# Kernel optimization log

Measured on AMD Instinct MI355X. Metric: run time of the kernel, lower is better.

The kernel has to match this reference:

```python
import jax, jax.numpy as jnp
import numpy as np

NUM_PHRASE = 8
HDIM = 256
NUM_HEADS = 8
NUM_LAYERS = 3
MIN_DIST = 2


def sine_pos(mask, num_feats, temperature=10000.0):
    # PositionEmbeddingSine (1D, DETR-style, normalize=False)
    B, L = mask.shape
    x_embed = jnp.cumsum(mask.astype(jnp.float32), axis=1)            # [B,L]
    dim_t = jnp.arange(num_feats, dtype=jnp.float32)
    dim_t = temperature ** (2.0 * jnp.floor(dim_t / 2.0) / num_feats)
    pos = x_embed[:, :, None] / dim_t                                  # [B,L,C]
    pos = jnp.stack([jnp.sin(pos[:, :, 0::2]), jnp.cos(pos[:, :, 1::2])], axis=3)
    return pos.reshape(B, L, num_feats)


def layer_norm(x, g, b, eps=1e-5):
    mu = jnp.mean(x, axis=-1, keepdims=True)
    var = jnp.mean((x - mu) ** 2, axis=-1, keepdims=True)
    return (x - mu) / jnp.sqrt(var + eps) * g + b


def mha(q, k, v, key_mask, in_w, in_b, out_w, out_b, nheads):
    # torch nn.MultiheadAttention (batch_first, eval/no-dropout), averaged attn weights
    B, Lq, C = q.shape
    Dh = C // nheads
    qp = (q @ in_w[:, :C] + in_b[:C]).reshape(B, Lq, nheads, Dh)
    kp = (k @ in_w[:, C:2 * C] + in_b[C:2 * C]).reshape(B, -1, nheads, Dh)
    vp = (v @ in_w[:, 2 * C:] + in_b[2 * C:]).reshape(B, -1, nheads, Dh)
    scores = jnp.einsum('bqhd,bkhd->bhqk', qp, kp) / jnp.sqrt(jnp.float32(Dh))
    scores = jnp.where(key_mask[:, None, None, :], scores, -jnp.inf)
    attn = jax.nn.softmax(scores, axis=-1)
    out = jnp.einsum('bhqk,bkhd->bqhd', attn, vp).reshape(B, Lq, C)
    return out @ out_w + out_b, jnp.mean(attn, axis=1)


def cross_attention(x, y, mask, qw, qb, kvw, kvb, inw, inb, ow, ob, g0, b0, lw, lb, g1, b1):
    C = x.shape[-1]
    q = x @ qw + qb
    kv = y @ kvw + kvb
    k, v = kv[..., :C], kv[..., C:]
    q_att, attn = mha(q, k, v, mask, inw, inb, ow, ob, NUM_HEADS)
    x = layer_norm(x + q_att, g0, b0)
    update = jax.nn.relu(x @ lw + lb)
    x = layer_norm(x + update, g1, b1)
    return x, attn


def _select_one(entropy_b, mask_b):
    # greedy highest-entropy selection with min-distance suppression (1D NMS)
    P, MD = NUM_PHRASE, MIN_DIST
    score = jnp.where(mask_b, entropy_b, -jnp.inf)
    order = jnp.argsort(-score).astype(jnp.int32)   # valid indices first, descending entropy

    def step(carry, idx):
        sel, cnt = carry
        dists = jnp.where(sel >= 0, jnp.abs(idx - sel), 1000000)
        ok = mask_b[idx] & (cnt < P) & (jnp.min(dists) >= MD)
        new_sel = jnp.where(ok, sel.at[jnp.minimum(cnt, P - 1)].set(idx), sel)
        return (new_sel, cnt + ok.astype(jnp.int32)), None

    init = (jnp.full((P,), -1, jnp.int32), jnp.int32(0))
    (sel, cnt), _ = jax.lax.scan(step, init, order)
    last = sel[jnp.maximum(cnt - 1, 0)]
    return jnp.where(jnp.arange(P) < cnt, sel, last)   # pad by repeating last


def phrase_generate(txt_emb, txt_mask, video_feats, video_mask,
                    word_proj_w, word_proj_b, video_proj_w, video_proj_b,
                    q_w, q_b, kv_w, kv_b, in_w, in_b, out_w, out_b,
                    ln0_g, ln0_b, lin_w, lin_b, ln1_g, ln1_b, eos_slot):
    B, L, C = txt_emb.shape
    word_emb = txt_emb[:, 1:]
    word_mask = txt_mask[:, 1:]
    word_pe = word_emb + sine_pos(word_mask, C)

    # word importance via video cross-attention entropy
    wp = word_pe @ word_proj_w + word_proj_b                      # [B,Lw,C]
    vp = video_feats @ video_proj_w + video_proj_b                # [B,T,C]
    sim = jnp.einsum('blc,btc->blt', wp, vp)                      # [B,Lw,T]
    sim = jnp.where(video_mask[:, None, :], sim, -jnp.inf)
    attn_weights = jax.nn.softmax(sim, axis=2)
    entropy = -jnp.sum(attn_weights * jnp.log(attn_weights + 1e-6), axis=2)  # [B,Lw]

    sel = jax.vmap(_select_one)(entropy, word_mask)               # [B,P] int32
    phrase_slot = jnp.take_along_axis(word_pe, sel[:, :, None], axis=1)      # [B,P,C]

    slot_sim = None
    for i in range(NUM_LAYERS):
        phrase_slot, slot_sim = cross_attention(
            phrase_slot, word_pe, word_mask,
            q_w[i], q_b[i], kv_w[i], kv_b[i], in_w[i], in_b[i], out_w[i], out_b[i],
            ln0_g[i], ln0_b[i], lin_w[i], lin_b[i], ln1_g[i], ln1_b[i])

    eos = jnp.broadcast_to(eos_slot, (B, 1, C))
    return phrase_slot, attn_weights, slot_sim, eos


def setup_inputs() -> dict:
    key = jax.random.key(0)
    ks = jax.random.split(key, 16)
    B, L, T, C, NL = 128, 257, 1024, HDIM, NUM_LAYERS
    s = 0.02
    inp = {
        'txt_emb': jax.random.normal(ks[0], (B, L, C), jnp.float32),
        'txt_mask': jnp.ones((B, L), jnp.bool_),
        'video_feats': jax.random.normal(ks[1], (B, T, C), jnp.float32),
        'video_mask': jnp.ones((B, T), jnp.bool_),
        'word_proj_w': jax.random.normal(ks[2], (C, C)) * s,
        'word_proj_b': jnp.zeros((C,)),
        'video_proj_w': jax.random.normal(ks[3], (C, C)) * s,
        'video_proj_b': jnp.zeros((C,)),
        'q_w': jax.random.normal(ks[4], (NL, C, C)) * s,
        'q_b': jnp.zeros((NL, C)),
        'kv_w': jax.random.normal(ks[5], (NL, C, 2 * C)) * s,
        'kv_b': jnp.zeros((NL, 2 * C)),
        'in_w': jax.random.normal(ks[6], (NL, C, 3 * C)) * s,
        'in_b': jnp.zeros((NL, 3 * C)),
        'out_w': jax.random.normal(ks[7], (NL, C, C)) * s,
        'out_b': jnp.zeros((NL, C)),
        'ln0_g': jnp.ones((NL, C)),
        'ln0_b': jnp.zeros((NL, C)),
        'lin_w': jax.random.normal(ks[8], (NL, C, C)) * s,
        'lin_b': jnp.zeros((NL, C)),
        'ln1_g': jnp.ones((NL, C)),
        'ln1_b': jnp.zeros((NL, C)),
        'eos_slot': jax.random.normal(ks[9], (1, 1, C)),
    }
    return inp


def reference(txt_emb, txt_mask, video_feats, video_mask,
              word_proj_w, word_proj_b, video_proj_w, video_proj_b,
              q_w, q_b, kv_w, kv_b, in_w, in_b, out_w, out_b,
              ln0_g, ln0_b, lin_w, lin_b, ln1_g, ln1_b, eos_slot):
    return phrase_generate(txt_emb, txt_mask, video_feats, video_mask,
                           word_proj_w, word_proj_b, video_proj_w, video_proj_b,
                           q_w, q_b, kv_w, kv_b, in_w, in_b, out_w, out_b,
                           ln0_g, ln0_b, lin_w, lin_b, ln1_g, ln1_b, eos_slot)
```

## Files before the change

kernel.cpp:

```cpp
#include <hip/hip_runtime.h>
#include <math.h>

#define BB 128
#define LFULL 257
#define LW 256
#define TT 1024
#define CC 256
#define NH 8
#define DHD 32
#define PP 8
#define NLAY 3

typedef __bf16 bf16x8 __attribute__((ext_vector_type(8)));
typedef __bf16 bf16x4 __attribute__((ext_vector_type(4)));
typedef float  f32x4  __attribute__((ext_vector_type(4)));

__device__ __forceinline__ float blockReduceSum(float v, volatile float* lds) {
#pragma unroll
    for (int m = 32; m >= 1; m >>= 1) v += __shfl_xor(v, m);
    __syncthreads();
    if ((threadIdx.x & 63) == 0) lds[threadIdx.x >> 6] = v;
    __syncthreads();
    return lds[0] + lds[1] + lds[2] + lds[3];
}
__device__ __forceinline__ float blockReduceMax(float v, volatile float* lds) {
#pragma unroll
    for (int m = 32; m >= 1; m >>= 1) v = fmaxf(v, __shfl_xor(v, m));
    __syncthreads();
    if ((threadIdx.x & 63) == 0) lds[threadIdx.x >> 6] = v;
    __syncthreads();
    return fmaxf(fmaxf(lds[0], lds[1]), fmaxf(lds[2], lds[3]));
}


__device__ __forceinline__ int ldsoff(int row, int col) {
    return ((row >> 6) << 11)
         + ((((row >> 4) & 3) << 2) + (col >> 3)) * 128
         + ((row & 15) << 3) + (col & 7);
}

template<int SPLIT, int B_F32, int OUT_SPLIT>
__global__ __launch_bounds__(256) void gemm_mfma(
    const __bf16* __restrict__ Ahi, const __bf16* __restrict__ Alo, int lda, long long sA,
    const void* __restrict__ Bhp, const void* __restrict__ Blp, int ldb, long long sB,
    const float* __restrict__ bias,
    float* __restrict__ Cf, __bf16* __restrict__ Chi, __bf16* __restrict__ Clo,
    int ldc, long long sC, int M, int N, int K)
{
    __shared__ __bf16 sAh[4096];
    __shared__ __bf16 sAl[SPLIT ? 4096 : 1];
    __shared__ __bf16 sBh[4096];
    __shared__ __bf16 sBl[SPLIT ? 4096 : 1];

    const int tid = threadIdx.x;
    const int n0 = blockIdx.x * 128;
    const int m0 = blockIdx.y * 128;
    const long long bz = blockIdx.z;
    const __bf16* Ah = Ahi + bz * sA;
    const __bf16* Al = SPLIT ? (Alo + bz * sA) : nullptr;

    const int wv = tid >> 6, lane = tid & 63;
    const int wm = (wv & 1) << 6, wn = (wv >> 1) << 6;
    const int lr = lane & 15, quad = lane >> 4;

    const int sr = tid >> 2;
    const int sc = (tid & 3) << 3;
    const int fr = tid >> 3;
    const int fc = (tid & 7) << 2;

    const int abase = ((wm >> 6) << 11) + (lane << 3);
    const int bbase = ((wn >> 6) << 11) + (lane << 3);

    f32x4 acc[4][4];
#pragma unroll
    for (int i = 0; i < 4; ++i)
#pragma unroll
        for (int j = 0; j < 4; ++j) acc[i][j] = (f32x4)(0.f);

    for (int k0 = 0; k0 < K; k0 += 32) {
#pragma unroll
        for (int j = 0; j < 2; ++j) {
            int row = sr + 64 * j;
            int off = ldsoff(row, sc);
            *(bf16x8*)&sAh[off] =
                *(const bf16x8*)&Ah[(long long)(m0 + row) * lda + k0 + sc];
            if constexpr (SPLIT)
                *(bf16x8*)&sAl[off] =
                    *(const bf16x8*)&Al[(long long)(m0 + row) * lda + k0 + sc];
        }
        if constexpr (B_F32) {
            const float* Bf = (const float*)Bhp + bz * sB;
#pragma unroll
            for (int j = 0; j < 4; ++j) {
                int row = fr + 32 * j;
                float4 f = *(const float4*)&Bf[(long long)(n0 + row) * ldb + k0 + fc];
                bf16x4 h4, l4;
                h4[0] = (__bf16)f.x; l4[0] = (__bf16)(f.x - (float)h4[0]);
                h4[1] = (__bf16)f.y; l4[1] = (__bf16)(f.y - (float)h4[1]);
                h4[2] = (__bf16)f.z; l4[2] = (__bf16)(f.z - (float)h4[2]);
                h4[3] = (__bf16)f.w; l4[3] = (__bf16)(f.w - (float)h4[3]);
                int off = ldsoff(row, fc);
                *(bf16x4*)&sBh[off] = h4;
                *(bf16x4*)&sBl[off] = l4;
            }
        } else {
            const __bf16* Bh = (const __bf16*)Bhp + bz * sB;
#pragma unroll
            for (int j = 0; j < 2; ++j) {
                int row = sr + 64 * j;
                int off = ldsoff(row, sc);
                *(bf16x8*)&sBh[off] =
                    *(const bf16x8*)&Bh[(long long)(n0 + row) * ldb + k0 + sc];
                if constexpr (SPLIT) {
                    const __bf16* Bl = (const __bf16*)Blp + bz * sB;
                    *(bf16x8*)&sBl[off] =
                        *(const bf16x8*)&Bl[(long long)(n0 + row) * ldb + k0 + sc];
                }
            }
        }
        __syncthreads();

        bf16x8 fah[4], fbh[4];
        bf16x8 fal[4], fbl[4];
#pragma unroll
        for (int i = 0; i < 4; ++i) {
            fah[i] = *(const bf16x8*)&sAh[abase + i * 512];
            fbh[i] = *(const bf16x8*)&sBh[bbase + i * 512];
            if constexpr (SPLIT) {
                fal[i] = *(const bf16x8*)&sAl[abase + i * 512];
                fbl[i] = *(const bf16x8*)&sBl[bbase + i * 512];
            }
        }
#pragma unroll
        for (int i = 0; i < 4; ++i)
#pragma unroll
            for (int j = 0; j < 4; ++j) {
                if constexpr (SPLIT) {
                    acc[i][j] = __builtin_amdgcn_mfma_f32_16x16x32_bf16(fal[i], fbh[j], acc[i][j], 0, 0, 0);
                    acc[i][j] = __builtin_amdgcn_mfma_f32_16x16x32_bf16(fah[i], fbl[j], acc[i][j], 0, 0, 0);
                }
                acc[i][j] = __builtin_amdgcn_mfma_f32_16x16x32_bf16(fah[i], fbh[j], acc[i][j], 0, 0, 0);
            }
        __syncthreads();
    }

#pragma unroll
    for (int i = 0; i < 4; ++i)
#pragma unroll
        for (int j = 0; j < 4; ++j) {
            int col = n0 + wn + j * 16 + lr;
            int row0 = m0 + wm + i * 16 + quad * 4;
            float bv = bias ? bias[col] : 0.f;
#pragma unroll
            for (int r = 0; r < 4; ++r) {
                float v = acc[i][j][r] + bv;
                long long off = (long long)(row0 + r) * ldc + col + bz * sC;
                if constexpr (OUT_SPLIT) {
                    __bf16 h = (__bf16)v;
                    Chi[off] = h;
                    Clo[off] = (__bf16)(v - (float)h);
                } else {
                    Cf[off] = v;
                }
            }
        }
}

#define GTS 64
#define GKT 16
#define GPAD 68

template<int TRANSB, int RELU, int TRANSC>
__global__ __launch_bounds__(256) void gemm_f32(
    const float* __restrict__ A, int lda, long long sA,
    const float* __restrict__ Bm, int ldb, long long sB,
    const float* __restrict__ bias,
    float* __restrict__ C, int ldc, long long sC,
    int M, int N, int K)
{
    __shared__ float As[GKT][GPAD];
    __shared__ float Bs[GKT][GPAD];
    const int tid = threadIdx.x;
    const int tx = tid & 15, ty = tid >> 4;
    const int n0 = blockIdx.x * GTS;
    const int m0 = blockIdx.y * GTS;
    const long long bz = blockIdx.z;
    const float* Ab = A + bz * sA;
    const float* Bb = Bm + bz * sB;
    float* Cb = C + bz * sC;

    const int lr = tid >> 2;
    const int lc = (tid & 3) << 2;
    const int br = tid >> 4;
    const int bc = (tid & 15) << 2;

    float acc[4][4] = {};

    for (int k0 = 0; k0 < K; k0 += GKT) {
        float4 a = *(const float4*)&Ab[(long long)(m0 + lr) * lda + k0 + lc];
        As[lc + 0][lr] = a.x; As[lc + 1][lr] = a.y;
        As[lc + 2][lr] = a.z; As[lc + 3][lr] = a.w;
        if (TRANSB) {
            float4 b = *(const float4*)&Bb[(long long)(n0 + lr) * ldb + k0 + lc];
            Bs[lc + 0][lr] = b.x; Bs[lc + 1][lr] = b.y;
            Bs[lc + 2][lr] = b.z; Bs[lc + 3][lr] = b.w;
        } else {
            float4 b = *(const float4*)&Bb[(long long)(k0 + br) * ldb + n0 + bc];
            *(float4*)&Bs[br][bc] = b;
        }
        __syncthreads();
#pragma unroll
        for (int k = 0; k < GKT; ++k) {
            float4 av = *(const float4*)&As[k][ty << 2];
            float4 bv = *(const float4*)&Bs[k][tx << 2];
            float ar[4] = {av.x, av.y, av.z, av.w};
            float brr[4] = {bv.x, bv.y, bv.z, bv.w};
#pragma unroll
            for (int i = 0; i < 4; ++i)
#pragma unroll
                for (int j = 0; j < 4; ++j)
                    acc[i][j] = fmaf(ar[i], brr[j], acc[i][j]);
        }
        __syncthreads();
    }

    float bbr[4] = {0.f, 0.f, 0.f, 0.f};
    if (bias) {
        float4 bb = *(const float4*)&bias[n0 + (tx << 2)];
        bbr[0] = bb.x; bbr[1] = bb.y; bbr[2] = bb.z; bbr[3] = bb.w;
    }
#pragma unroll
    for (int i = 0; i < 4; ++i) {
#pragma unroll
        for (int j = 0; j < 4; ++j) {
            float o = acc[i][j] + bbr[j];
            if (RELU) o = fmaxf(o, 0.f);
            if (TRANSC)
                Cb[(long long)(n0 + (tx << 2) + j) * ldc + m0 + (ty << 2) + i] = o;
            else
                Cb[(long long)(m0 + (ty << 2) + i) * ldc + n0 + (tx << 2) + j] = o;
        }
    }
}


__global__ __launch_bounds__(256) void cumsum_kernel(
    const int* __restrict__ tm, int* __restrict__ cums)
{
    int b = blockIdx.x, c = threadIdx.x;
    int lane = c & 63;
    int v = (tm[(long long)b * LFULL + 1 + c] != 0) ? 1 : 0;
#pragma unroll
    for (int off = 1; off < 64; off <<= 1) {
        int t = __shfl_up(v, off);
        if (lane >= off) v += t;
    }
    __shared__ int wsum[4];
    if (lane == 63) wsum[c >> 6] = v;
    __syncthreads();
    int w = c >> 6, add = 0;
    for (int i = 0; i < w; ++i) add += wsum[i];
    cums[b * LW + c] = v + add;
}

__global__ __launch_bounds__(256) void pe_table_kernel(float* __restrict__ petab)
{
    int n = blockIdx.x;
    int c = threadIdx.x;
    int i2 = c & ~1;
    float freq = powf(10000.0f, (float)i2 / (float)CC);
    float arg = (float)n / freq;
    petab[n * CC + c] = (c & 1) ? cosf(arg) : sinf(arg);
}

__global__ __launch_bounds__(256) void word_pe2_kernel(
    const float* __restrict__ te, const int* __restrict__ cums,
    const float* __restrict__ petab,
    __bf16* __restrict__ whi, __bf16* __restrict__ wlo)
{
    int g = blockIdx.x * 256 + threadIdx.x;
    int c0 = (g & 63) << 2;
    int l  = (g >> 6) & 255;
    int b  = g >> 14;
    int cnt = cums[b * LW + l];
    float4 s = *(const float4*)&te[((long long)(b * LFULL + 1 + l)) * CC + c0];
    float4 p = *(const float4*)&petab[cnt * CC + c0];
    float v0 = s.x + p.x, v1 = s.y + p.y, v2 = s.z + p.z, v3 = s.w + p.w;
    bf16x4 h, lo;
    h[0] = (__bf16)v0; lo[0] = (__bf16)(v0 - (float)h[0]);
    h[1] = (__bf16)v1; lo[1] = (__bf16)(v1 - (float)h[1]);
    h[2] = (__bf16)v2; lo[2] = (__bf16)(v2 - (float)h[2]);
    h[3] = (__bf16)v3; lo[3] = (__bf16)(v3 - (float)h[3]);
    long long o = ((long long)(b * LW + l)) * CC + c0;
    *(bf16x4*)&whi[o] = h;
    *(bf16x4*)&wlo[o] = lo;
}

__global__ __launch_bounds__(256) void split_transpose_kernel(
    const float* __restrict__ W, __bf16* __restrict__ hi, __bf16* __restrict__ lo)
{
    int n = blockIdx.x, k = threadIdx.x;
    float v = W[(long long)k * CC + n];
    __bf16 h = (__bf16)v;
    hi[(long long)n * CC + k] = h;
    lo[(long long)n * CC + k] = (__bf16)(v - (float)h);
}
__global__ __launch_bounds__(256) void split_plain_kernel(
    const float* __restrict__ W, __bf16* __restrict__ hi, __bf16* __restrict__ lo)
{
    int g = blockIdx.x * 256 + threadIdx.x;
    float v = W[g];
    __bf16 h = (__bf16)v;
    hi[g] = h;
    lo[g] = (__bf16)(v - (float)h);
}
__global__ __launch_bounds__(256) void cvt_bf16_kernel(
    const float* __restrict__ src, __bf16* __restrict__ dst)
{
    int g = blockIdx.x * 256 + threadIdx.x;
    dst[g] = (__bf16)src[g];
}

__global__ __launch_bounds__(256) void softmax_entropy_kernel(
    float* __restrict__ attn, const int* __restrict__ vmask,
    float* __restrict__ ent)
{
    __shared__ float lds[4];
    long long row = blockIdx.x;
    int b = blockIdx.x >> 8;
    float* p = attn + row * TT;
    const int* m = vmask + (long long)b * TT;
    int t4 = threadIdx.x * 4;
    float4 v = *(const float4*)&p[t4];
    int4 mm4 = *(const int4*)&m[t4];
    float x[4];
    x[0] = mm4.x ? v.x : -INFINITY;
    x[1] = mm4.y ? v.y : -INFINITY;
    x[2] = mm4.z ? v.z : -INFINITY;
    x[3] = mm4.w ? v.w : -INFINITY;
    float mx = fmaxf(fmaxf(x[0], x[1]), fmaxf(x[2], x[3]));
    mx = blockReduceMax(mx, lds);
    float e[4];
    float ps = 0.f;
#pragma unroll
    for (int j = 0; j < 4; ++j) { e[j] = expf(x[j] - mx); ps += e[j]; }
    float sum = blockReduceSum(ps, lds);
    float q[4];
    float ce = 0.f;
#pragma unroll
    for (int j = 0; j < 4; ++j) {
        q[j] = e[j] / sum;
        ce += q[j] * logf(q[j] + 1e-6f);
    }
    ce = blockReduceSum(ce, lds);
    *(float4*)&p[t4] = make_float4(q[0], q[1], q[2], q[3]);
    if (threadIdx.x == 0) ent[row] = -ce;
}

__global__ __launch_bounds__(256) void select_kernel(
    const float* __restrict__ ent, const int* __restrict__ tm,
    int* __restrict__ sel)
{
    int b = blockIdx.x;
    int l = threadIdx.x;
    __shared__ float sc[LW];
    __shared__ int ord[LW];
    __shared__ unsigned char mk[LW];
    mk[l] = (tm[(long long)b * LFULL + 1 + l] != 0);
    sc[l] = mk[l] ? ent[(long long)b * LW + l] : -INFINITY;
    __syncthreads();
    float mys = sc[l];
    int r = 0;
    for (int j = 0; j < LW; ++j) {
        float s = sc[j];
        r += (s > mys) || (s == mys && j < l);
    }
    ord[r] = l;
    __syncthreads();
    if (l == 0) {
        int chosen[PP];
        int cnt = 0;
        for (int t = 0; t < LW; ++t) {
            int idx = ord[t];
            if (!mk[idx]) continue;
            if (cnt >= PP) break;
            bool ok = true;
            for (int s2 = 0; s2 < cnt; ++s2) {
                int d = idx - chosen[s2];
                if (d < 0) d = -d;
                if (d < 2) ok = false;
            }
            if (ok) chosen[cnt++] = idx;
        }
        int last = (cnt > 0) ? chosen[cnt - 1] : -1;
        for (int p = 0; p < PP; ++p)
            sel[b * PP + p] = (p < cnt) ? chosen[p] : last;
    }
}

__global__ __launch_bounds__(256) void gather_kernel(
    const __bf16* __restrict__ whi, const __bf16* __restrict__ wlo,
    const int* __restrict__ sel, float* __restrict__ x0)
{
    int g = blockIdx.x * 256 + threadIdx.x;
    int b = g >> 11;
    int p = (g >> 8) & 7;
    int c = g & 255;
    int idx = sel[b * PP + p];
    if (idx < 0) idx = 0;
    long long off = ((long long)b * LW + idx) * CC + c;
    x0[g] = (float)whi[off] + (float)wlo[off];
}

__global__ __launch_bounds__(256) void eff_bias_kernel(
    const float* __restrict__ q_b, const float* __restrict__ kv_b,
    const float* __restrict__ in_w, const float* __restrict__ in_b,
    float* __restrict__ BQE_all, float* __restrict__ bkv3)
{
    int i = blockIdx.x / 3;
    int role = blockIdx.x % 3;
    int n = threadIdx.x;
    const float* inw = in_w + (long long)i * 196608;
    const float* inb = in_b + (long long)i * 768;
    const float* srcb;
    int co;
    float* dst;
    if (role == 0)      { srcb = q_b + i * 256;        co = 0;   dst = BQE_all + i * 256; }
    else if (role == 1) { srcb = kv_b + i * 512;       co = 256; dst = bkv3 + i * 512; }
    else                { srcb = kv_b + i * 512 + 256; co = 512; dst = bkv3 + i * 512 + 256; }
    float s = inb[co + n];
    for (int k = 0; k < CC; ++k)
        s = fmaf(srcb[k], inw[(long long)k * 768 + co + n], s);
    dst[n] = s;
}

__global__ __launch_bounds__(256) void attn_scores_kernel(
    const float* __restrict__ qp, const float* __restrict__ KV,
    const int* __restrict__ tm, float* __restrict__ attn)
{
    int b = blockIdx.x, h = blockIdx.y;
    int tid = threadIdx.x;
    __shared__ float qs[PP][DHD];
    __shared__ float sc[PP][LW];
    __shared__ float mxs[PP], sms[PP];
    {
        int q = tid >> 5, d = tid & 31;
        qs[q][d] = qp[((long long)(b * PP + q)) * CC + h * DHD + d];
    }
    __syncthreads();
    const float* kr = KV + ((long long)(b * LW + tid)) * 512 + h * DHD;
    float kreg[DHD];
#pragma unroll
    for (int j = 0; j < 8; ++j) {
        float4 f = *(const float4*)&kr[j * 4];
        kreg[j * 4 + 0] = f.x; kreg[j * 4 + 1] = f.y;
        kreg[j * 4 + 2] = f.z; kreg[j * 4 + 3] = f.w;
    }
    bool mk = tm[(long long)b * LFULL + 1 + tid] != 0;
#pragma unroll
    for (int q = 0; q < PP; ++q) {
        float s = 0.f;
#pragma unroll
        for (int d = 0; d < DHD; ++d) s = fmaf(qs[q][d], kreg[d], s);
        sc[q][tid] = mk ? s * 0.17677669529663687f : -INFINITY;
    }
    __syncthreads();
    {
        int q = tid >> 5, j = tid & 31;
        float m = -INFINITY;
        for (int kk = j; kk < LW; kk += 32) m = fmaxf(m, sc[q][kk]);
#pragma unroll
        for (int mm = 16; mm >= 1; mm >>= 1) m = fmaxf(m, __shfl_xor(m, mm, 32));
        float s = 0.f;
        for (int kk = j; kk < LW; kk += 32) s += expf(sc[q][kk] - m);
#pragma unroll
        for (int mm = 16; mm >= 1; mm >>= 1) s += __shfl_xor(s, mm, 32);
        if (j == 0) { mxs[q] = m; sms[q] = s; }
    }
    __syncthreads();
#pragma unroll
    for (int q = 0; q < PP; ++q) {
        float pv = expf(sc[q][tid] - mxs[q]) / sms[q];
        attn[(((long long)(b * NH + h)) * PP + q) * LW + tid] = pv;
    }
}

__global__ __launch_bounds__(256) void attn_out_kernel(
    const float* __restrict__ attn, const float* __restrict__ KV,
    float* __restrict__ aout)
{
    int b = blockIdx.x, q = blockIdx.y;
    int c = threadIdx.x, h = c >> 5;
    __shared__ float att[NH][LW];
#pragma unroll
    for (int hh = 0; hh < NH; ++hh)
        att[hh][c] = attn[(((long long)(b * NH + hh)) * PP + q) * LW + c];
    __syncthreads();
    const float* vpb = KV + ((long long)b * LW) * 512 + 256 + c;
    float acc = 0.f;
#pragma unroll 8
    for (int k = 0; k < LW; ++k)
        acc = fmaf(att[h][k], vpb[(long long)k * 512], acc);
    aout[((long long)(b * PP + q)) * CC + c] = acc;
}

__global__ __launch_bounds__(256) void slot_sim_kernel(
    const float* __restrict__ attn, float* __restrict__ outs)
{
    int b = blockIdx.x, q = blockIdx.y, k = threadIdx.x;
    float s = 0.f;
#pragma unroll
    for (int h = 0; h < NH; ++h)
        s += attn[(((long long)(b * NH + h)) * PP + q) * LW + k];
    outs[((long long)(b * PP + q)) * LW + k] = s * 0.125f;
}

__global__ __launch_bounds__(256) void ln_residual_kernel(
    const float* __restrict__ xin, const float* __restrict__ add,
    const float* __restrict__ g, const float* __restrict__ bta,
    float* __restrict__ out)
{
    __shared__ float lds[4];
    int r = blockIdx.x, c = threadIdx.x;
    long long idx = (long long)r * CC + c;
    float v = xin[idx] + add[idx];
    float s = blockReduceSum(v, lds);
    float mu = s * (1.0f / (float)CC);
    float d = v - mu;
    float var = blockReduceSum(d * d, lds) * (1.0f / (float)CC);
    out[idx] = d / sqrtf(var + 1e-5f) * g[c] + bta[c];
}

__global__ __launch_bounds__(256) void eos_kernel(
    const float* __restrict__ eos, float* __restrict__ outp)
{
    outp[(long long)blockIdx.x * CC + threadIdx.x] = eos[threadIdx.x];
}

extern "C" void kernel_launch(void* const* d_in, const int* in_sizes, int n_in,
                              void* d_out, int out_size, void* d_ws, size_t ws_size,
                              hipStream_t stream) {
    const float* txt_emb     = (const float*)d_in[0];
    const int*   txt_mask    = (const int*)d_in[1];
    const float* video_feats = (const float*)d_in[2];
    const int*   video_mask  = (const int*)d_in[3];
    const float* word_proj_w = (const float*)d_in[4];
    const float* word_proj_b = (const float*)d_in[5];
    const float* video_proj_w = (const float*)d_in[6];
    const float* q_w   = (const float*)d_in[8];
    const float* q_b   = (const float*)d_in[9];
    const float* kv_w  = (const float*)d_in[10];
    const float* kv_b  = (const float*)d_in[11];
    const float* in_w  = (const float*)d_in[12];
    const float* in_b  = (const float*)d_in[13];
    const float* out_w = (const float*)d_in[14];
    const float* out_b = (const float*)d_in[15];
    const float* ln0_g = (const float*)d_in[16];
    const float* ln0_b = (const float*)d_in[17];
    const float* lin_w = (const float*)d_in[18];
    const float* lin_b = (const float*)d_in[19];
    const float* ln1_g = (const float*)d_in[20];
    const float* ln1_b = (const float*)d_in[21];
    const float* eos_slot = (const float*)d_in[22];

    float* ws = (float*)d_ws;
    __bf16* wpe_hi = (__bf16*)(ws + 0LL);
    __bf16* wpe_lo = (__bf16*)(ws + 4194304LL);
    __bf16* wp_hi  = (__bf16*)(ws + 8388608LL);
    __bf16* wp_lo  = (__bf16*)(ws + 12582912LL);
    __bf16* U_hi   = (__bf16*)(ws + 16777216LL);
    __bf16* U_lo   = (__bf16*)(ws + 20971520LL);
    float*  KV     = ws + 8388608LL;
    float* ent     = ws + 25165824LL;
    int*   sel     = (int*)(ws + 25198592LL);
    float* x0      = ws + 25199616LL;
    float* x1      = ws + 25461760LL;
    float* xmid    = ws + 25723904LL;
    float* qp      = ws + 25986048LL;
    float* attnw   = ws + 26248192LL;
    float* aout    = ws + 28345344LL;
    float* qatt    = ws + 28607488LL;
    float* upd     = ws + 28869632LL;
    float* WQE_all = ws + 29131776LL;
    float* BQE_all = ws + 29328384LL;
    float* WT3f    = ws + 29329152LL;
    __bf16* WT3    = (__bf16*)(ws + 29722368LL);
    float* bkv3    = ws + 29918976LL;
    __bf16* WPT_hi = (__bf16*)(ws + 29920512LL);
    __bf16* WPT_lo = (__bf16*)(ws + 29953280LL);
    __bf16* VPS_hi = (__bf16*)(ws + 29986048LL);
    __bf16* VPS_lo = (__bf16*)(ws + 30018816LL);

    int*   cums  = (int*)(ws + 8388608LL);
    float* petab = ws + 8421376LL;

    float* outp     = (float*)d_out;
    float* out_ps   = outp;
    float* out_attn = outp + 262144LL;
    float* out_slot = outp + 33816576LL;
    float* out_eos  = outp + 34078720LL;

    cumsum_kernel<<<dim3(BB), dim3(256), 0, stream>>>(txt_mask, cums);
    pe_table_kernel<<<dim3(257), dim3(256), 0, stream>>>(petab);
    word_pe2_kernel<<<dim3(8192), dim3(256), 0, stream>>>(txt_emb, cums, petab, wpe_hi, wpe_lo);
    split_transpose_kernel<<<dim3(256), dim3(256), 0, stream>>>(word_proj_w, WPT_hi, WPT_lo);
    split_plain_kernel<<<dim3(256), dim3(256), 0, stream>>>(video_proj_w, VPS_hi, VPS_lo);
    gemm_mfma<1,0,1><<<dim3(2,256,1), dim3(256), 0, stream>>>(
        wpe_hi, wpe_lo, 256, 0, WPT_hi, WPT_lo, 256, 0, word_proj_b,
        nullptr, wp_hi, wp_lo, 256, 0, 32768, 256, 256);
    gemm_mfma<1,0,1><<<dim3(2,256,1), dim3(256), 0, stream>>>(
        wp_hi, wp_lo, 256, 0, VPS_hi, VPS_lo, 256, 0, nullptr,
        nullptr, U_hi, U_lo, 256, 0, 32768, 256, 256);
    gemm_mfma<1,1,0><<<dim3(8,2,BB), dim3(256), 0, stream>>>(
        U_hi, U_lo, 256, 65536LL, video_feats, nullptr, 256, 262144LL, nullptr,
        out_attn, nullptr, nullptr, 1024, 262144LL, 256, 1024, 256);
    softmax_entropy_kernel<<<dim3(32768), dim3(256), 0, stream>>>(out_attn, video_mask, ent);
    select_kernel<<<dim3(BB), dim3(256), 0, stream>>>(ent, txt_mask, sel);
    gather_kernel<<<dim3(1024), dim3(256), 0, stream>>>(wpe_hi, wpe_lo, sel, x0);

    gemm_f32<0,0,0><<<dim3(4,4,3), dim3(256), 0, stream>>>(
        q_w,256,65536LL, in_w,768,196608LL, nullptr, WQE_all,256,65536LL, 256,256,256);
    gemm_f32<0,0,1><<<dim3(4,4,3), dim3(256), 0, stream>>>(
        kv_w,512,131072LL, in_w+256,768,196608LL, nullptr, WT3f,256,131072LL, 256,256,256);
    gemm_f32<0,0,1><<<dim3(4,4,3), dim3(256), 0, stream>>>(
        kv_w+256,512,131072LL, in_w+512,768,196608LL, nullptr, WT3f+65536,256,131072LL, 256,256,256);
    eff_bias_kernel<<<dim3(9), dim3(256), 0, stream>>>(q_b, kv_b, in_w, in_b, BQE_all, bkv3);
    cvt_bf16_kernel<<<dim3(1536), dim3(256), 0, stream>>>(WT3f, (__bf16*)WT3);

    float* X = x0;
    for (int i = 0; i < NLAY; ++i) {
        const float* ow  = out_w + (long long)i * 65536;
        const float* ob  = out_b + (long long)i * 256;
        const float* g0  = ln0_g + (long long)i * 256;
        const float* b0  = ln0_b + (long long)i * 256;
        const float* lw  = lin_w + (long long)i * 65536;
        const float* lb  = lin_b + (long long)i * 256;
        const float* g1  = ln1_g + (long long)i * 256;
        const float* b1  = ln1_b + (long long)i * 256;

        gemm_mfma<0,0,0><<<dim3(4,256,1), dim3(256), 0, stream>>>(
            wpe_hi, nullptr, 256, 0, WT3 + (long long)i * 131072, nullptr, 256, 0,
            bkv3 + i * 512, KV, nullptr, nullptr, 512, 0, 32768, 512, 256);

        gemm_f32<0,0,0><<<dim3(4,16,1), dim3(256), 0, stream>>>(
            X,256,0, WQE_all + (long long)i*65536,256,0, BQE_all + i*256, qp,256,0, 1024,256,256);

        attn_scores_kernel<<<dim3(BB,NH), dim3(256), 0, stream>>>(qp, KV, txt_mask, attnw);
        attn_out_kernel<<<dim3(BB,PP), dim3(256), 0, stream>>>(attnw, KV, aout);
        if (i == NLAY - 1)
            slot_sim_kernel<<<dim3(BB,PP), dim3(256), 0, stream>>>(attnw, out_slot);

        gemm_f32<0,0,0><<<dim3(4,16,1), dim3(256), 0, stream>>>(
            aout,256,0, ow,256,0, ob, qatt,256,0, 1024,256,256);
        ln_residual_kernel<<<dim3(1024), dim3(256), 0, stream>>>(X, qatt, g0, b0, xmid);
        gemm_f32<0,1,0><<<dim3(4,16,1), dim3(256), 0, stream>>>(
            xmid,256,0, lw,256,0, lb, upd,256,0, 1024,256,256);
        float* Xout = (i == NLAY - 1) ? out_ps : ((X == x0) ? x1 : x0);
        ln_residual_kernel<<<dim3(1024), dim3(256), 0, stream>>>(xmid, upd, g1, b1, Xout);
        X = Xout;
    }
    eos_kernel<<<dim3(BB), dim3(256), 0, stream>>>(eos_slot, out_eos);
}
```

Baseline: 914.9 us.

## Use 512-thread blocks in MFMA GEMM with 8 waves per 128x128 tile

The bf16 MFMA GEMM now launches 512 threads per block, so 8 waves each compute a 64x32 sub-tile instead of 4 waves each computing 64x64. Each thread loads one row-chunk of A and B per k-step instead of two, and the fp32 B path converts 8 values per thread. The goal is more waves in flight to hide latency and a smaller per-thread accumulator and register footprint. The trade-off is more barrier participants and a lower MFMA-to-LDS-read ratio per wave.

Measured after the change: 894.1 us. -2.3%, faster.

```diff
diff --git a/kernel.cpp b/kernel.cpp
--- a/kernel.cpp
+++ b/kernel.cpp
@@ -40,7 +40,7 @@
 }
 
 template<int SPLIT, int B_F32, int OUT_SPLIT>
-__global__ __launch_bounds__(256) void gemm_mfma(
+__global__ __launch_bounds__(512, 4) void gemm_mfma(
     const __bf16* __restrict__ Ahi, const __bf16* __restrict__ Alo, int lda, long long sA,
     const void* __restrict__ Bhp, const void* __restrict__ Blp, int ldb, long long sB,
     const float* __restrict__ bias,
@@ -60,81 +60,79 @@
     const __bf16* Al = SPLIT ? (Alo + bz * sA) : nullptr;
 
     const int wv = tid >> 6, lane = tid & 63;
-    const int wm = (wv & 1) << 6, wn = (wv >> 1) << 6;
+    const int wm = (wv & 1) << 6;
+    const int wn = (wv >> 1) << 5;
     const int lr = lane & 15, quad = lane >> 4;
 
     const int sr = tid >> 2;
     const int sc = (tid & 3) << 3;
-    const int fr = tid >> 3;
-    const int fc = (tid & 7) << 2;
 
     const int abase = ((wm >> 6) << 11) + (lane << 3);
-    const int bbase = ((wn >> 6) << 11) + (lane << 3);
-
-    f32x4 acc[4][4];
+    const int bbase = ((wn >> 6) << 11) + (((wn >> 4) & 3) << 9) + (lane << 3);
+
+    f32x4 acc[4][2];
 #pragma unroll
     for (int i = 0; i < 4; ++i)
 #pragma unroll
-        for (int j = 0; j < 4; ++j) acc[i][j] = (f32x4)(0.f);
+        for (int j = 0; j < 2; ++j) acc[i][j] = (f32x4)(0.f);
 
     for (int k0 = 0; k0 < K; k0 += 32) {
-#pragma unroll
-        for (int j = 0; j < 2; ++j) {
-            int row = sr + 64 * j;
-            int off = ldsoff(row, sc);
+        {
+            int off = ldsoff(sr, sc);
             *(bf16x8*)&sAh[off] =
-                *(const bf16x8*)&Ah[(long long)(m0 + row) * lda + k0 + sc];
+                *(const bf16x8*)&Ah[(long long)(m0 + sr) * lda + k0 + sc];
             if constexpr (SPLIT)
                 *(bf16x8*)&sAl[off] =
-                    *(const bf16x8*)&Al[(long long)(m0 + row) * lda + k0 + sc];
+                    *(const bf16x8*)&Al[(long long)(m0 + sr) * lda + k0 + sc];
         }
         if constexpr (B_F32) {
             const float* Bf = (const float*)Bhp + bz * sB;
-#pragma unroll
-            for (int j = 0; j < 4; ++j) {
-                int row = fr + 32 * j;
-                float4 f = *(const float4*)&Bf[(long long)(n0 + row) * ldb + k0 + fc];
-                bf16x4 h4, l4;
-                h4[0] = (__bf16)f.x; l4[0] = (__bf16)(f.x - (float)h4[0]);
-                h4[1] = (__bf16)f.y; l4[1] = (__bf16)(f.y - (float)h4[1]);
-                h4[2] = (__bf16)f.z; l4[2] = (__bf16)(f.z - (float)h4[2]);
-                h4[3] = (__bf16)f.w; l4[3] = (__bf16)(f.w - (float)h4[3]);
-                int off = ldsoff(row, fc);
-                *(bf16x4*)&sBh[off] = h4;
-                *(bf16x4*)&sBl[off] = l4;
-            }
+            const float* src = &Bf[(long long)(n0 + sr) * ldb + k0 + sc];
+            float4 f0 = *(const float4*)&src[0];
+            float4 f1 = *(const float4*)&src[4];
+            bf16x8 h8, l8;
+            h8[0] = (__bf16)f0.x; l8[0] = (__bf16)(f0.x - (float)h8[0]);
+            h8[1] = (__bf16)f0.y; l8[1] = (__bf16)(f0.y - (float)h8[1]);
+            h8[2] = (__bf16)f0.z; l8[2] = (__bf16)(f0.z - (float)h8[2]);
+            h8[3] = (__bf16)f0.w; l8[3] = (__bf16)(f0.w - (float)h8[3]);
+            h8[4] = (__bf16)f1.x; l8[4] = (__bf16)(f1.x - (float)h8[4]);
+            h8[5] = (__bf16)f1.y; l8[5] = (__bf16)(f1.y - (float)h8[5]);
+            h8[6] = (__bf16)f1.z; l8[6] = (__bf16)(f1.z - (float)h8[6]);
+            h8[7] = (__bf16)f1.w; l8[7] = (__bf16)(f1.w - (float)h8[7]);
+            int off = ldsoff(sr, sc);
+            *(bf16x8*)&sBh[off] = h8;
+            *(bf16x8*)&sBl[off] = l8;
         } else {
             const __bf16* Bh = (const __bf16*)Bhp + bz * sB;
-#pragma unroll
-            for (int j = 0; j < 2; ++j) {
-                int row = sr + 64 * j;
-                int off = ldsoff(row, sc);
-                *(bf16x8*)&sBh[off] =
-                    *(const bf16x8*)&Bh[(long long)(n0 + row) * ldb + k0 + sc];
-                if constexpr (SPLIT) {
-                    const __bf16* Bl = (const __bf16*)Blp + bz * sB;
-                    *(bf16x8*)&sBl[off] =
-                        *(const bf16x8*)&Bl[(long long)(n0 + row) * ldb + k0 + sc];
-                }
+            int off = ldsoff(sr, sc);
+            *(bf16x8*)&sBh[off] =
+                *(const bf16x8*)&Bh[(long long)(n0 + sr) * ldb + k0 + sc];
+            if constexpr (SPLIT) {
+                const __bf16* Bl = (const __bf16*)Blp + bz * sB;
+                *(bf16x8*)&sBl[off] =
+                    *(const bf16x8*)&Bl[(long long)(n0 + sr) * ldb + k0 + sc];
             }
         }
         __syncthreads();
 
-        bf16x8 fah[4], fbh[4];
-        bf16x8 fal[4], fbl[4];
+        bf16x8 fah[4], fbh[2];
+        bf16x8 fal[4], fbl[2];
 #pragma unroll
         for (int i = 0; i < 4; ++i) {
             fah[i] = *(const bf16x8*)&sAh[abase + i * 512];
-            fbh[i] = *(const bf16x8*)&sBh[bbase + i * 512];
-            if constexpr (SPLIT) {
+            if constexpr (SPLIT)
                 fal[i] = *(const bf16x8*)&sAl[abase + i * 512];
-                fbl[i] = *(const bf16x8*)&sBl[bbase + i * 512];
-            }
+        }
+#pragma unroll
+        for (int j = 0; j < 2; ++j) {
+            fbh[j] = *(const bf16x8*)&sBh[bbase + j * 512];
+            if constexpr (SPLIT)
+                fbl[j] = *(const bf16x8*)&sBl[bbase + j * 512];
         }
 #pragma unroll
         for (int i = 0; i < 4; ++i)
 #pragma unroll
-            for (int j = 0; j < 4; ++j) {
+            for (int j = 0; j < 2; ++j) {
                 if constexpr (SPLIT) {
                     acc[i][j] = __builtin_amdgcn_mfma_f32_16x16x32_bf16(fal[i], fbh[j], acc[i][j], 0, 0, 0);
                     acc[i][j] = __builtin_amdgcn_mfma_f32_16x16x32_bf16(fah[i], fbl[j], acc[i][j], 0, 0, 0);
@@ -147,7 +145,7 @@
 #pragma unroll
     for (int i = 0; i < 4; ++i)
 #pragma unroll
-        for (int j = 0; j < 4; ++j) {
+        for (int j = 0; j < 2; ++j) {
             int col = n0 + wn + j * 16 + lr;
             int row0 = m0 + wm + i * 16 + quad * 4;
             float bv = bias ? bias[col] : 0.f;
@@ -605,13 +603,13 @@
     word_pe2_kernel<<<dim3(8192), dim3(256), 0, stream>>>(txt_emb, cums, petab, wpe_hi, wpe_lo);
     split_transpose_kernel<<<dim3(256), dim3(256), 0, stream>>>(word_proj_w, WPT_hi, WPT_lo);
     split_plain_kernel<<<dim3(256), dim3(256), 0, stream>>>(video_proj_w, VPS_hi, VPS_lo);
-    gemm_mfma<1,0,1><<<dim3(2,256,1), dim3(256), 0, stream>>>(
+    gemm_mfma<1,0,1><<<dim3(2,256,1), dim3(512), 0, stream>>>(
         wpe_hi, wpe_lo, 256, 0, WPT_hi, WPT_lo, 256, 0, word_proj_b,
         nullptr, wp_hi, wp_lo, 256, 0, 32768, 256, 256);
-    gemm_mfma<1,0,1><<<dim3(2,256,1), dim3(256), 0, stream>>>(
+    gemm_mfma<1,0,1><<<dim3(2,256,1), dim3(512), 0, stream>>>(
         wp_hi, wp_lo, 256, 0, VPS_hi, VPS_lo, 256, 0, nullptr,
         nullptr, U_hi, U_lo, 256, 0, 32768, 256, 256);
-    gemm_mfma<1,1,0><<<dim3(8,2,BB), dim3(256), 0, stream>>>(
+    gemm_mfma<1,1,0><<<dim3(8,2,BB), dim3(512), 0, stream>>>(
         U_hi, U_lo, 256, 65536LL, video_feats, nullptr, 256, 262144LL, nullptr,
         out_attn, nullptr, nullptr, 1024, 262144LL, 256, 1024, 256);
     softmax_entropy_kernel<<<dim3(32768), dim3(256), 0, stream>>>(out_attn, video_mask, ent);
@@ -638,7 +636,7 @@
         const float* g1  = ln1_g + (long long)i * 256;
         const float* b1  = ln1_b + (long long)i * 256;
 
-        gemm_mfma<0,0,0><<<dim3(4,256,1), dim3(256), 0, stream>>>(
+        gemm_mfma<0,0,0><<<dim3(4,256,1), dim3(512), 0, stream>>>(
             wpe_hi, nullptr, 256, 0, WT3 + (long long)i * 131072, nullptr, 256, 0,
             bkv3 + i * 512, KV, nullptr, nullptr, 512, 0, 32768, 512, 256);
 
```
